# Optimization experiments

Hardware: AMD Instinct MI355X
Metric: run time of the kernel (lower is better)

Reference implementation:

```python
import jax, jax.numpy as jnp
import numpy as np

N_NODES = 50000
N_EDGES = 1600000
IN_CH = 512
HID_CH = 256


def _gcn_conv(x, edge_index, W, b):
    """PyG-style GCNConv: add self-loops, symmetric normalization, x@W then aggregate."""
    n = x.shape[0]
    loop = jnp.arange(n, dtype=edge_index.dtype)
    src = jnp.concatenate([edge_index[0], loop])  # [E+N]
    dst = jnp.concatenate([edge_index[1], loop])  # [E+N]
    deg = jax.ops.segment_sum(jnp.ones_like(dst, dtype=x.dtype), dst, num_segments=n)
    dinv = jnp.where(deg > 0, jax.lax.rsqrt(deg), 0.0)
    norm = dinv[src] * dinv[dst]  # [E+N]
    h = x @ W  # transform first (smaller feature dim for aggregation)
    msg = h[src] * norm[:, None]  # [E+N, F_out]
    out = jax.ops.segment_sum(msg, dst, num_segments=n)
    return out + b


def setup_inputs() -> dict:
    key = jax.random.key(0)
    ks = jax.random.split(key, 8)
    x = jax.random.normal(ks[0], (N_NODES, IN_CH), dtype=jnp.float32)
    edge_index = jax.random.randint(ks[1], (2, N_EDGES), 0, N_NODES, dtype=jnp.int32)
    W1 = jax.random.normal(ks[2], (IN_CH, HID_CH), dtype=jnp.float32) * (1.0 / np.sqrt(IN_CH))
    b1 = jnp.zeros((HID_CH,), dtype=jnp.float32)
    W2 = jax.random.normal(ks[3], (HID_CH, 32), dtype=jnp.float32) * (1.0 / np.sqrt(HID_CH))
    b2 = jnp.zeros((32,), dtype=jnp.float32)
    Wl = jax.random.normal(ks[4], (32, 2), dtype=jnp.float32) * (1.0 / np.sqrt(32))
    bl = jnp.zeros((2,), dtype=jnp.float32)
    return {"x": x, "edge_index": edge_index, "W1": W1, "b1": b1,
            "W2": W2, "b2": b2, "Wl": Wl, "bl": bl}


def reference(x, edge_index, W1, b1, W2, b2, Wl, bl):
    h = _gcn_conv(x, edge_index, W1, b1)
    h = jax.nn.relu(h)
    h = _gcn_conv(h, edge_index, W2, b2)
    # F.dropout(training=...) treated as identity (eval-mode reference)
    logits = h @ Wl + bl
    return jax.nn.log_softmax(logits, axis=1)
```

## Files before the change

kernel.cpp:

```cpp
#include <hip/hip_runtime.h>
#include <hip/hip_bf16.h>
#include <stdint.h>

#define NN 50000
#define NE 1600000
#define CIN 512
#define CH1 256
#define CH2 32

#define NBUCK 196
#define CAP 10240
#define CAP2 16384
#define ECH 4096
#define NCH 391

typedef __bf16 bf16_t;
typedef __attribute__((ext_vector_type(2))) __bf16 bf16x2;
typedef __attribute__((ext_vector_type(8))) __bf16 bf16x8;
typedef __attribute__((ext_vector_type(4))) float f32x4;
typedef __attribute__((ext_vector_type(2))) float f32x2;
typedef __attribute__((ext_vector_type(4))) uint32_t u32x4;

__device__ inline float blo(uint32_t v) { return __uint_as_float(v << 16); }
__device__ inline float bhi(uint32_t v) { return __uint_as_float(v & 0xffff0000u); }
__device__ inline uint32_t pk2(float a, float b) {
  bf16x2 p; p[0] = (__bf16)a; p[1] = (__bf16)b; return *(uint32_t*)&p;
}

__global__ __launch_bounds__(256) void k_hist(const int* __restrict__ dst,
                                              int* __restrict__ counts) {
  __shared__ int h[256];
  int blk = blockIdx.x, t = threadIdx.x;
  int e0 = blk * ECH;
  int ce = NE - e0; if (ce > ECH) ce = ECH;
  h[t] = 0;
  __syncthreads();
  for (int k = t; k < ce; k += 256) atomicAdd(&h[dst[e0 + k] >> 8], 1);
  __syncthreads();
  if (t < NBUCK) counts[blk * NBUCK + t] = h[t];
}

__global__ __launch_bounds__(512) void k_scanb(const int* __restrict__ counts,
                                               int* __restrict__ offs,
                                               int* __restrict__ bcnt) {
  __shared__ int l[512];
  int b = blockIdx.x, t = threadIdx.x;
  int v = (t < NCH) ? counts[t * NBUCK + b] : 0;
  int x = v;
  l[t] = x;
  __syncthreads();
  for (int off = 1; off < 512; off <<= 1) {
    int u = (t >= off) ? l[t - off] : 0;
    __syncthreads();
    x += u; l[t] = x;
    __syncthreads();
  }
  if (t < NCH) offs[t * NBUCK + b] = b * CAP + (x - v);
  if (t == 511) bcnt[b] = x;
}

__global__ __launch_bounds__(256) void k_bin(const int* __restrict__ src,
    const int* __restrict__ dst, const int* __restrict__ offs,
    uint32_t* __restrict__ binned) {
  __shared__ int h[256], lbase[256], lcnt[256], offsL[256];
  __shared__ uint32_t lstage[ECH];
  int blk = blockIdx.x, t = threadIdx.x;
  int e0 = blk * ECH;
  int ce = NE - e0; if (ce > ECH) ce = ECH;
  h[t] = 0; lcnt[t] = 0;
  if (t < NBUCK) offsL[t] = offs[blk * NBUCK + t];
  __syncthreads();
  for (int k = t; k < ce; k += 256) atomicAdd(&h[dst[e0 + k] >> 8], 1);
  __syncthreads();
  int v = h[t], x = v;
  lbase[t] = x;
  __syncthreads();
  for (int off = 1; off < 256; off <<= 1) {
    int u = (t >= off) ? lbase[t - off] : 0;
    __syncthreads();
    x += u; lbase[t] = x;
    __syncthreads();
  }
  lbase[t] = x - v;
  __syncthreads();
  for (int k = t; k < ce; k += 256) {
    int d = dst[e0 + k], s = src[e0 + k];
    int bkt = d >> 8;
    int p = lbase[bkt] + atomicAdd(&lcnt[bkt], 1);
    lstage[p] = ((uint32_t)bkt << 24) | ((uint32_t)(d & 255) << 16) | (uint32_t)s;
  }
  __syncthreads();
  for (int j = t; j < ce; j += 256) {
    uint32_t e = lstage[j];
    int bkt = e >> 24;
    binned[offsL[bkt] + (j - lbase[bkt])] = e & 0x00ffffffu;
  }
}

__global__ __launch_bounds__(256) void k_build(const uint32_t* __restrict__ binned,
    const int* __restrict__ bcnt, int* __restrict__ rowptr2, int* __restrict__ deg2,
    float* __restrict__ dinv, uint16_t* __restrict__ csrs) {
  __shared__ int hist[256], prow[256], lcnt[256];
  __shared__ int tot_s;
  __shared__ uint32_t c2[CAP2];
  int b = blockIdx.x, t = threadIdx.x;
  int count = bcnt[b];
  hist[t] = 0; lcnt[t] = 0;
  __syncthreads();
  const uint32_t* bb = binned + (size_t)b * CAP;
  for (int j = t; j < count; j += 256) atomicAdd(&hist[bb[j] >> 16], 1);
  __syncthreads();
  int node = b * 256 + t;
  int deg = hist[t];
  int pdeg = (node < NN) ? ((deg + 16) & ~15) : 0;
  int x = pdeg;
  prow[t] = x;
  __syncthreads();
  for (int off = 1; off < 256; off <<= 1) {
    int u = (t >= off) ? prow[t - off] : 0;
    __syncthreads();
    x += u; prow[t] = x;
    __syncthreads();
  }
  int start = x - pdeg;
  prow[t] = start;
  if (t == 255) tot_s = x;
  if (node < NN) {
    rowptr2[node] = b * CAP2 + start;
    deg2[node] = pdeg;
    dinv[node] = 1.0f / sqrtf((float)(deg + 1));
    c2[start + deg] = (uint32_t)node;
    for (int k = deg + 1; k < pdeg; ++k)
      c2[start + k] = (uint32_t)NN;
  }
  __syncthreads();
  for (int j = t; j < count; j += 256) {
    uint32_t e = bb[j];
    int dl = e >> 16;
    int p = prow[dl] + atomicAdd(&lcnt[dl], 1);
    c2[p] = e & 0xffffu;
  }
  __syncthreads();
  int tot = tot_s;
  uint16_t* co = csrs + (size_t)b * CAP2;
  for (int j = t; j < tot; j += 256) co[j] = (uint16_t)c2[j];
}

__global__ void k_prep_w(const float* __restrict__ W1, const float* __restrict__ W2,
                         bf16_t* __restrict__ w1t, bf16_t* __restrict__ w2t,
                         uint32_t* __restrict__ h1p_u32, uint32_t* __restrict__ h2b_u32) {
  int i = blockIdx.x * 256 + threadIdx.x;
  if (i < CIN * CH1) {
    int n = i >> 9, k = i & 511;
    w1t[i] = (__bf16)W1[k * CH1 + n];
  }
  if (i < CH1 * CH2) {
    int oc = i >> 8, k = i & 255;
    w2t[i] = (__bf16)W2[k * CH2 + oc];
  }
  if (blockIdx.x == 0) {
    int t = threadIdx.x;
    if (t < 128) {
      int p = t >> 4;
      h1p_u32[((size_t)p * (NN + 1) + NN) * 16 + (t & 15)] = 0;
    } else if (t < 144) {
      h2b_u32[(size_t)NN * 16 + (t - 128)] = 0;
    }
  }
}

#define BM 128
#define BN 128
#define BK 64

__global__ __launch_bounds__(256) void k_gemm1(const float* __restrict__ X,
                                               const bf16_t* __restrict__ BT,
                                               const float* __restrict__ dinv,
                                               bf16_t* __restrict__ h1p) {
  __shared__ __align__(16) bf16_t ldsA[2][BM * BK];
  __shared__ __align__(16) bf16_t ldsB[2][BN * BK];
  const int tid = threadIdx.x;
  const int lane = tid & 63;
  const int wid = tid >> 6;
  const int tm = blockIdx.x, tn = blockIdx.y;
  const int wm = wid >> 1, wn = wid & 1;

  f32x4 acc[4][4] = {};
  float4 ra[4], rb[4];

  auto loadA = [&](int kt) {
#pragma unroll
    for (int q = 0; q < 4; ++q) {
      int idx16 = q * 256 + tid;
      int r = idx16 >> 3, cw = idx16 & 7;
      int grow = tm * BM + r;
      grow = grow < NN ? grow : NN - 1;
      const float* ga = X + (size_t)grow * CIN + kt * BK + cw * 8;
      ra[q] = *(const float4*)ga;
      rb[q] = *(const float4*)(ga + 4);
    }
  };
  auto writeA = [&](int buf) {
#pragma unroll
    for (int q = 0; q < 4; ++q) {
      int idx16 = q * 256 + tid;
      int r = idx16 >> 3, cw = idx16 & 7;
      bf16x8 o;
      o[0] = (__bf16)ra[q].x; o[1] = (__bf16)ra[q].y;
      o[2] = (__bf16)ra[q].z; o[3] = (__bf16)ra[q].w;
      o[4] = (__bf16)rb[q].x; o[5] = (__bf16)rb[q].y;
      o[6] = (__bf16)rb[q].z; o[7] = (__bf16)rb[q].w;
      *(bf16x8*)&ldsA[buf][r * 64 + ((cw ^ (r & 7)) << 3)] = o;
    }
  };
  auto stageB = [&](int buf, int kt) {
#pragma unroll
    for (int t = 0; t < 4; ++t) {
      int o = t * 4096 + tid * 16;
      int r = o >> 7, cw = (o >> 4) & 7;
      int lc = cw ^ (r & 7);
      const bf16_t* gb = BT + (size_t)(tn * BN + r) * CIN + kt * BK + lc * 8;
      __builtin_amdgcn_global_load_lds(
          (const __attribute__((address_space(1))) void*)gb,
          (__attribute__((address_space(3))) void*)&ldsB[buf][(t * 4096 + wid * 1024) >> 1],
          16, 0, 0);
    }
  };

  loadA(0);
  stageB(0, 0);
  writeA(0);
  __syncthreads();
  int cur = 0;
  for (int kt = 0; kt < CIN / BK; ++kt) {
    if (kt + 1 < CIN / BK) { loadA(kt + 1); stageB(cur ^ 1, kt + 1); }
#pragma unroll
    for (int ks = 0; ks < 2; ++ks) {
      bf16x8 af[4], bfr[4];
#pragma unroll
      for (int m = 0; m < 4; ++m) {
        int row = wm * 64 + m * 16 + (lane & 15);
        int kc = ks * 4 + (lane >> 4);
        af[m] = *(const bf16x8*)&ldsA[cur][row * 64 + ((kc ^ (row & 7)) << 3)];
      }
#pragma unroll
      for (int n = 0; n < 4; ++n) {
        int col = wn * 64 + n * 16 + (lane & 15);
        int kc = ks * 4 + (lane >> 4);
        bfr[n] = *(const bf16x8*)&ldsB[cur][col * 64 + ((kc ^ (col & 7)) << 3)];
      }
#pragma unroll
      for (int m = 0; m < 4; ++m)
#pragma unroll
        for (int n = 0; n < 4; ++n)
          acc[m][n] = __builtin_amdgcn_mfma_f32_16x16x32_bf16(af[m], bfr[n], acc[m][n], 0, 0, 0);
    }
    if (kt + 1 < CIN / BK) writeA(cur ^ 1);
    __syncthreads();
    cur ^= 1;
  }

#pragma unroll
  for (int m = 0; m < 4; ++m) {
#pragma unroll
    for (int r = 0; r < 4; ++r) {
      int grow = tm * BM + wm * 64 + m * 16 + (lane >> 4) * 4 + r;
      if (grow < NN) {
        float dv = dinv[grow];
#pragma unroll
        for (int n = 0; n < 4; ++n) {
          int gcol = tn * BN + wn * 64 + n * 16 + (lane & 15);
          int plane = gcol >> 5, pc = gcol & 31;
          h1p[(size_t)plane * ((NN + 1) * 32) + (size_t)grow * 32 + pc] =
              (__bf16)(dv * acc[m][n][r]);
        }
      }
    }
  }
}

__global__ __launch_bounds__(256) void k_agg1(const uint32_t* __restrict__ h1p,
    const int* __restrict__ rowptr2, const int* __restrict__ deg2,
    const uint16_t* __restrict__ csrs, const float* __restrict__ dinv,
    const float* __restrict__ bias, uint32_t* __restrict__ hrp) {
  const int s = blockIdx.x & 7;
  const int lane = threadIdx.x & 63;
  const int wid = threadIdx.x >> 6;
  int i = (blockIdx.x >> 3) * 64 + wid * 16 + (lane >> 2);
  const bool valid = i < NN;
  i = valid ? i : NN - 1;
  const int cl = lane & 3;
  const int grp = lane & 60;
  const int cb = cl << 4;
  const char* __restrict__ Pb = (const char*)(h1p + (size_t)s * ((NN + 1) * 16));

  f32x2 a0 = {0.f, 0.f}, a1 = {0.f, 0.f}, a2 = {0.f, 0.f}, a3 = {0.f, 0.f};
  const int base = rowptr2[i];
  const int pdeg = deg2[i];
  uint32_t ent = __builtin_nontemporal_load((const uint32_t*)&csrs[base + cl * 2]);
  for (int b0 = 0; b0 < pdeg; b0 += 8) {
    uint32_t ent_n = __builtin_nontemporal_load(
        (const uint32_t*)&csrs[base + b0 + 8 + cl * 2]);
    int s0 = (int)(ent & 0xffffu) << 6;
    int s1 = (int)(ent >> 16) << 6;
#pragma unroll
    for (int e = 0; e < 8; ++e) {
      int off = __shfl((e & 1) ? s1 : s0, grp + (e >> 1)) + cb;
      u32x4 v = *(const u32x4*)(Pb + off);
      f32x2 f0 = {blo(v.x), bhi(v.x)};
      f32x2 f1 = {blo(v.y), bhi(v.y)};
      f32x2 f2 = {blo(v.z), bhi(v.z)};
      f32x2 f3 = {blo(v.w), bhi(v.w)};
      a0 += f0; a1 += f1; a2 += f2; a3 += f3;
    }
    ent = ent_n;
  }
  float di = dinv[i];
  float4 b0v = *(const float4*)&bias[s * 32 + cl * 8];
  float4 b1v = *(const float4*)&bias[s * 32 + cl * 8 + 4];
  u32x4 o;
  o.x = pk2(fmaxf(di * a0.x + b0v.x, 0.f), fmaxf(di * a0.y + b0v.y, 0.f));
  o.y = pk2(fmaxf(di * a1.x + b0v.z, 0.f), fmaxf(di * a1.y + b0v.w, 0.f));
  o.z = pk2(fmaxf(di * a2.x + b1v.x, 0.f), fmaxf(di * a2.y + b1v.y, 0.f));
  o.w = pk2(fmaxf(di * a3.x + b1v.z, 0.f), fmaxf(di * a3.y + b1v.w, 0.f));
  if (valid)
    __builtin_nontemporal_store(o,
        (u32x4*)&hrp[((size_t)s * NN + i) * 16 + cl * 4]);
}

__global__ __launch_bounds__(256) void k_gemm2(const bf16_t* __restrict__ hrp,
    const bf16_t* __restrict__ w2t, const float* __restrict__ dinv,
    bf16_t* __restrict__ h2b) {
  const int lane = threadIdx.x & 63;
  const int gw = blockIdx.x * 4 + (threadIdx.x >> 6);
  const int r0 = gw * 16;
  if (r0 >= NN) return;
  int arow = r0 + (lane & 15);
  arow = arow < NN ? arow : NN - 1;
  const int kc = lane >> 4;
  f32x4 acc0 = {}, acc1 = {};
#pragma unroll
  for (int kb = 0; kb < 8; ++kb) {
    bf16x8 a  = *(const bf16x8*)&hrp[(size_t)kb * (NN * 32) + (size_t)arow * 32 + kc * 8];
    bf16x8 b0 = *(const bf16x8*)&w2t[(size_t)(lane & 15) * CH1 + kb * 32 + kc * 8];
    bf16x8 b1 = *(const bf16x8*)&w2t[(size_t)(16 + (lane & 15)) * CH1 + kb * 32 + kc * 8];
    acc0 = __builtin_amdgcn_mfma_f32_16x16x32_bf16(a, b0, acc0, 0, 0, 0);
    acc1 = __builtin_amdgcn_mfma_f32_16x16x32_bf16(a, b1, acc1, 0, 0, 0);
  }
#pragma unroll
  for (int r = 0; r < 4; ++r) {
    int rr = r0 + (lane >> 4) * 4 + r;
    if (rr < NN) {
      float dv = dinv[rr];
      h2b[(size_t)rr * CH2 + (lane & 15)]      = (__bf16)(dv * acc0[r]);
      h2b[(size_t)rr * CH2 + 16 + (lane & 15)] = (__bf16)(dv * acc1[r]);
    }
  }
}

__global__ __launch_bounds__(256) void k_agg2(const uint32_t* __restrict__ h2b,
    const int* __restrict__ rowptr2, const int* __restrict__ deg2,
    const uint16_t* __restrict__ csrs, const float* __restrict__ dinv,
    const float* __restrict__ b2, const float* __restrict__ Wl,
    const float* __restrict__ bl, float* __restrict__ out) {
  const int lane = threadIdx.x & 63;
  const int wid = threadIdx.x >> 6;
  int i = blockIdx.x * 64 + wid * 16 + (lane >> 2);
  const bool valid = i < NN;
  i = valid ? i : NN - 1;
  const int cl = lane & 3;
  const int grp = lane & 60;
  const int cb = cl << 4;
  const char* __restrict__ Pb = (const char*)h2b;

  f32x2 a0 = {0.f, 0.f}, a1 = {0.f, 0.f}, a2 = {0.f, 0.f}, a3 = {0.f, 0.f};
  const int base = rowptr2[i];
  const int pdeg = deg2[i];
  uint32_t ent = __builtin_nontemporal_load((const uint32_t*)&csrs[base + cl * 2]);
  for (int b0 = 0; b0 < pdeg; b0 += 8) {
    uint32_t ent_n = __builtin_nontemporal_load(
        (const uint32_t*)&csrs[base + b0 + 8 + cl * 2]);
    int s0 = (int)(ent & 0xffffu) << 6;
    int s1 = (int)(ent >> 16) << 6;
#pragma unroll
    for (int e = 0; e < 8; ++e) {
      int off = __shfl((e & 1) ? s1 : s0, grp + (e >> 1)) + cb;
      u32x4 v = *(const u32x4*)(Pb + off);
      f32x2 f0 = {blo(v.x), bhi(v.x)};
      f32x2 f1 = {blo(v.y), bhi(v.y)};
      f32x2 f2 = {blo(v.z), bhi(v.z)};
      f32x2 f3 = {blo(v.w), bhi(v.w)};
      a0 += f0; a1 += f1; a2 += f2; a3 += f3;
    }
    ent = ent_n;
  }
  float di = dinv[i];
  float vv[8];
  vv[0] = di * a0.x + b2[cl * 8 + 0]; vv[1] = di * a0.y + b2[cl * 8 + 1];
  vv[2] = di * a1.x + b2[cl * 8 + 2]; vv[3] = di * a1.y + b2[cl * 8 + 3];
  vv[4] = di * a2.x + b2[cl * 8 + 4]; vv[5] = di * a2.y + b2[cl * 8 + 5];
  vv[6] = di * a3.x + b2[cl * 8 + 6]; vv[7] = di * a3.y + b2[cl * 8 + 7];
  float lp0 = 0.f, lp1 = 0.f;
  const float2* Wl2 = (const float2*)Wl;
#pragma unroll
  for (int k = 0; k < 8; ++k) {
    float2 wl = Wl2[cl * 8 + k];
    lp0 += vv[k] * wl.x;
    lp1 += vv[k] * wl.y;
  }
  lp0 += __shfl_xor(lp0, 1); lp0 += __shfl_xor(lp0, 2);
  lp1 += __shfl_xor(lp1, 1); lp1 += __shfl_xor(lp1, 2);
  if (valid && cl == 0) {
    float l0 = lp0 + bl[0], l1 = lp1 + bl[1];
    float m = fmaxf(l0, l1);
    float lse = m + logf(expf(l0 - m) + expf(l1 - m));
    float2 o; o.x = l0 - lse; o.y = l1 - lse;
    *(float2*)&out[i * 2] = o;
  }
}

extern "C" void kernel_launch(void* const* d_in, const int* in_sizes, int n_in,
                              void* d_out, int out_size, void* d_ws, size_t ws_size,
                              hipStream_t stream) {
  const float* x  = (const float*)d_in[0];
  const int*   ei = (const int*)d_in[1];
  const float* W1 = (const float*)d_in[2];
  const float* b1 = (const float*)d_in[3];
  const float* W2 = (const float*)d_in[4];
  const float* b2 = (const float*)d_in[5];
  const float* Wl = (const float*)d_in[6];
  const float* bl = (const float*)d_in[7];
  float* out = (float*)d_out;

  const int* src = ei;
  const int* dst = ei + NE;

  uint8_t* w = (uint8_t*)d_ws;
  auto alloc = [&](size_t bytes) { void* p = w; w += (bytes + 255) & ~(size_t)255; return p; };
  int*      counts = (int*)alloc((size_t)NCH * NBUCK * 4);
  int*      offs   = (int*)alloc((size_t)NCH * NBUCK * 4);
  int*      bcnt   = (int*)alloc((size_t)NBUCK * 4);
  uint32_t* binned = (uint32_t*)alloc((size_t)NBUCK * CAP * 4);
  uint16_t* csrs   = (uint16_t*)alloc((size_t)NBUCK * CAP2 * 2);
  int*      rowptr2= (int*)alloc((size_t)NN * 4);
  int*      deg2   = (int*)alloc((size_t)NN * 4);
  float*    dinv   = (float*)alloc((size_t)NN * 4);
  bf16_t*   w1t    = (bf16_t*)alloc((size_t)CIN * CH1 * 2);
  bf16_t*   w2t    = (bf16_t*)alloc((size_t)CH1 * CH2 * 2);
  bf16_t*   h1p    = (bf16_t*)alloc((size_t)(NN + 1) * CH1 * 2);
  bf16_t*   hrp    = (bf16_t*)alloc((size_t)NN * CH1 * 2);
  bf16_t*   h2b    = (bf16_t*)alloc((size_t)(NN + 1) * CH2 * 2);

  k_hist <<<NCH, 256, 0, stream>>>(dst, counts);
  k_scanb<<<NBUCK, 512, 0, stream>>>(counts, offs, bcnt);
  k_bin  <<<NCH, 256, 0, stream>>>(src, dst, offs, binned);
  k_build<<<NBUCK, 256, 0, stream>>>(binned, bcnt, rowptr2, deg2, dinv, csrs);

  k_prep_w<<<(CIN * CH1 + 255) / 256, 256, 0, stream>>>(W1, W2, w1t, w2t,
                                                        (uint32_t*)h1p, (uint32_t*)h2b);

  dim3 g1((NN + BM - 1) / BM, CH1 / BN);
  k_gemm1<<<g1, 256, 0, stream>>>(x, w1t, dinv, h1p);

  int nb = (NN + 63) / 64;
  k_agg1<<<nb * 8, 256, 0, stream>>>((const uint32_t*)h1p, rowptr2, deg2,
                                     csrs, dinv, b1, (uint32_t*)hrp);
  k_gemm2<<<(NN / 16 + 3) / 4, 256, 0, stream>>>(hrp, w2t, dinv, h2b);
  k_agg2<<<nb, 256, 0, stream>>>((const uint32_t*)h2b, rowptr2, deg2, csrs,
                                 dinv, b2, Wl, bl, out);
}
```

Baseline: 235.8 us.

## Retile gemm1 to full-width N tiles and simplify edge binning scatter

The first GEMM now uses 64-row by 256-column tiles, so each block covers all output channels and the fp32 X rows are read and converted to bf16 only once instead of twice. Each of the four waves computes a 64x64 slab, and B staging now loads the whole 256-row weight tile per K step, which doubles the shared memory used for B. Separately, k_bin drops its local histogram, prefix scan and shared-memory staging pass and writes each edge straight to global memory via an atomic counter. This removes several barriers but makes the global writes uncoalesced and the order of edges within a bucket nondeterministic.

```diff
diff --git a/kernel.cpp b/kernel.cpp
--- a/kernel.cpp
+++ b/kernel.cpp
@@ -62,38 +62,18 @@
 __global__ __launch_bounds__(256) void k_bin(const int* __restrict__ src,
     const int* __restrict__ dst, const int* __restrict__ offs,
     uint32_t* __restrict__ binned) {
-  __shared__ int h[256], lbase[256], lcnt[256], offsL[256];
-  __shared__ uint32_t lstage[ECH];
+  __shared__ int lcnt[256], offsL[256];
   int blk = blockIdx.x, t = threadIdx.x;
   int e0 = blk * ECH;
   int ce = NE - e0; if (ce > ECH) ce = ECH;
-  h[t] = 0; lcnt[t] = 0;
+  lcnt[t] = 0;
   if (t < NBUCK) offsL[t] = offs[blk * NBUCK + t];
-  __syncthreads();
-  for (int k = t; k < ce; k += 256) atomicAdd(&h[dst[e0 + k] >> 8], 1);
-  __syncthreads();
-  int v = h[t], x = v;
-  lbase[t] = x;
-  __syncthreads();
-  for (int off = 1; off < 256; off <<= 1) {
-    int u = (t >= off) ? lbase[t - off] : 0;
-    __syncthreads();
-    x += u; lbase[t] = x;
-    __syncthreads();
-  }
-  lbase[t] = x - v;
   __syncthreads();
   for (int k = t; k < ce; k += 256) {
     int d = dst[e0 + k], s = src[e0 + k];
     int bkt = d >> 8;
-    int p = lbase[bkt] + atomicAdd(&lcnt[bkt], 1);
-    lstage[p] = ((uint32_t)bkt << 24) | ((uint32_t)(d & 255) << 16) | (uint32_t)s;
-  }
-  __syncthreads();
-  for (int j = t; j < ce; j += 256) {
-    uint32_t e = lstage[j];
-    int bkt = e >> 24;
-    binned[offsL[bkt] + (j - lbase[bkt])] = e & 0x00ffffffu;
+    int p = atomicAdd(&lcnt[bkt], 1);
+    binned[offsL[bkt] + p] = ((uint32_t)(d & 255) << 16) | (uint32_t)s;
   }
 }
 
@@ -169,8 +149,8 @@
   }
 }
 
-#define BM 128
-#define BN 128
+#define BM 64
+#define BN 256
 #define BK 64
 
 __global__ __launch_bounds__(256) void k_gemm1(const float* __restrict__ X,
@@ -182,15 +162,14 @@
   const int tid = threadIdx.x;
   const int lane = tid & 63;
   const int wid = tid >> 6;
-  const int tm = blockIdx.x, tn = blockIdx.y;
-  const int wm = wid >> 1, wn = wid & 1;
+  const int tm = blockIdx.x;
 
   f32x4 acc[4][4] = {};
-  float4 ra[4], rb[4];
+  float4 ra[2], rb[2];
 
   auto loadA = [&](int kt) {
 #pragma unroll
-    for (int q = 0; q < 4; ++q) {
+    for (int q = 0; q < 2; ++q) {
       int idx16 = q * 256 + tid;
       int r = idx16 >> 3, cw = idx16 & 7;
       int grow = tm * BM + r;
@@ -202,7 +181,7 @@
   };
   auto writeA = [&](int buf) {
 #pragma unroll
-    for (int q = 0; q < 4; ++q) {
+    for (int q = 0; q < 2; ++q) {
       int idx16 = q * 256 + tid;
       int r = idx16 >> 3, cw = idx16 & 7;
       bf16x8 o;
@@ -215,11 +194,11 @@
   };
   auto stageB = [&](int buf, int kt) {
 #pragma unroll
-    for (int t = 0; t < 4; ++t) {
+    for (int t = 0; t < 8; ++t) {
       int o = t * 4096 + tid * 16;
       int r = o >> 7, cw = (o >> 4) & 7;
       int lc = cw ^ (r & 7);
-      const bf16_t* gb = BT + (size_t)(tn * BN + r) * CIN + kt * BK + lc * 8;
+      const bf16_t* gb = BT + (size_t)r * CIN + kt * BK + lc * 8;
       __builtin_amdgcn_global_load_lds(
           (const __attribute__((address_space(1))) void*)gb,
           (__attribute__((address_space(3))) void*)&ldsB[buf][(t * 4096 + wid * 1024) >> 1],
@@ -239,13 +218,13 @@
       bf16x8 af[4], bfr[4];
 #pragma unroll
       for (int m = 0; m < 4; ++m) {
-        int row = wm * 64 + m * 16 + (lane & 15);
+        int row = m * 16 + (lane & 15);
         int kc = ks * 4 + (lane >> 4);
         af[m] = *(const bf16x8*)&ldsA[cur][row * 64 + ((kc ^ (row & 7)) << 3)];
       }
 #pragma unroll
       for (int n = 0; n < 4; ++n) {
-        int col = wn * 64 + n * 16 + (lane & 15);
+        int col = wid * 64 + n * 16 + (lane & 15);
         int kc = ks * 4 + (lane >> 4);
         bfr[n] = *(const bf16x8*)&ldsB[cur][col * 64 + ((kc ^ (col & 7)) << 3)];
       }
@@ -264,12 +243,12 @@
   for (int m = 0; m < 4; ++m) {
 #pragma unroll
     for (int r = 0; r < 4; ++r) {
-      int grow = tm * BM + wm * 64 + m * 16 + (lane >> 4) * 4 + r;
+      int grow = tm * BM + m * 16 + (lane >> 4) * 4 + r;
       if (grow < NN) {
         float dv = dinv[grow];
 #pragma unroll
         for (int n = 0; n < 4; ++n) {
-          int gcol = tn * BN + wn * 64 + n * 16 + (lane & 15);
+          int gcol = wid * 64 + n * 16 + (lane & 15);
           int plane = gcol >> 5, pc = gcol & 31;
           h1p[(size_t)plane * ((NN + 1) * 32) + (size_t)grow * 32 + pc] =
               (__bf16)(dv * acc[m][n][r]);
@@ -459,7 +438,7 @@
   k_prep_w<<<(CIN * CH1 + 255) / 256, 256, 0, stream>>>(W1, W2, w1t, w2t,
                                                         (uint32_t*)h1p, (uint32_t*)h2b);
 
-  dim3 g1((NN + BM - 1) / BM, CH1 / BN);
+  dim3 g1((NN + BM - 1) / BM);
   k_gemm1<<<g1, 256, 0, stream>>>(x, w1t, dinv, h1p);
 
   int nb = (NN + 63) / 64;
```

After: 222.7 us. 1.06x faster.
